# Kernel optimization log

Measured on AMD Instinct MI355X. Metric: run time of the kernel, lower is better.

Reference implementation:

```python
import jax, jax.numpy as jnp
import numpy as np

B, T, V, H, E, MAX_OOV = 128, 200, 50257, 256, 128, 50


def setup_inputs() -> dict:
    key = jax.random.key(0)
    ks = jax.random.split(key, 17)
    s = 0.05  # param scale
    return {
        "decoder_input": jax.random.randint(ks[0], (B, 1), 0, V),
        "encoder_outputs": jax.random.normal(ks[1], (B, T, 2 * H), jnp.float32),
        "encoder_idxs": jax.random.randint(ks[2], (B, T), 0, V),
        "prev_state": jax.random.normal(ks[3], (1, B, H), jnp.float32),
        "selective_read": jax.random.normal(ks[4], (B, 1, 2 * H), jnp.float32) * s,
        "step": 1,
        "emb": jax.random.normal(ks[5], (V, E), jnp.float32) * s,
        "W_ih": jax.random.normal(ks[6], (3 * H, E + 2 * H), jnp.float32) * s,
        "W_hh": jax.random.normal(ks[7], (3 * H, H), jnp.float32) * s,
        "b_ih": jax.random.normal(ks[8], (3 * H,), jnp.float32) * s,
        "b_hh": jax.random.normal(ks[9], (3 * H,), jnp.float32) * s,
        "Wi_w": jax.random.normal(ks[10], (H, 2 * H), jnp.float32) * s,
        "Wi_b": jax.random.normal(ks[11], (H,), jnp.float32) * s,
        "Wg_w": jax.random.normal(ks[12], (V, H), jnp.float32) * s,
        "Wg_b": jax.random.normal(ks[13], (V,), jnp.float32) * s,
        "Wc_w": jax.random.normal(ks[14], (H, 2 * H), jnp.float32) * s,
        "Wc_b": jax.random.normal(ks[15], (H,), jnp.float32) * s,
    }


def _gru_cell(x, h, W_ih, W_hh, b_ih, b_hh):
    # torch GRUCell math, gate order r,z,n
    gi = x @ W_ih.T + b_ih
    gh = h @ W_hh.T + b_hh
    i_r, i_z, i_n = jnp.split(gi, 3, axis=-1)
    h_r, h_z, h_n = jnp.split(gh, 3, axis=-1)
    r = jax.nn.sigmoid(i_r + h_r)
    z = jax.nn.sigmoid(i_z + h_z)
    n = jnp.tanh(i_n + r * h_n)
    return (1.0 - z) * n + z * h


def reference(decoder_input, encoder_outputs, encoder_idxs, prev_state, selective_read,
              step, emb, W_ih, W_hh, b_ih, b_hh, Wi_w, Wi_b, Wg_w, Wg_b, Wc_w, Wc_b):
    dtype = encoder_outputs.dtype
    if step == 0:
        prev_state = (encoder_outputs[:, -1] @ Wi_w.T + Wi_b)[None]      # 1,B,H
        selective_read = jnp.zeros((B, 1, 2 * H), dtype)
    embedded = emb[decoder_input[:, 0]]                                   # B,E
    gru_in = jnp.concatenate([selective_read[:, 0], embedded], axis=-1)   # B,2H+E
    decode_hidden = _gru_cell(gru_in, prev_state[0], W_ih, W_hh, b_ih, b_hh)  # B,H

    score_g = decode_hidden @ Wg_w.T + Wg_b                               # B,V
    enc_proj = jnp.tanh(jnp.einsum('bte,he->bth', encoder_outputs, Wc_w) + Wc_b)  # B,T,H
    score_c = jnp.tanh(jnp.einsum('bth,bh->bt', enc_proj, decode_hidden))         # B,T
    score_c = score_c + jnp.where(encoder_idxs == 0, -10000.0, 0.0).astype(dtype)

    probs = jax.nn.softmax(jnp.concatenate([score_g, score_c], axis=1), axis=1)   # B,V+T
    prob_g, prob_c = probs[:, :V], probs[:, V:]
    prob_g = jnp.concatenate([prob_g, jnp.full((B, MAX_OOV), 1e-4, dtype)], axis=1)  # B,V+oov

    # copy-distribution aggregation: scatter-add prob_c by vocab id (replaces one-hot bmm)
    prob_c_to_g = jnp.zeros((B, V + MAX_OOV), dtype).at[
        jnp.arange(B)[:, None], encoder_idxs].add(prob_c)
    prob_out = (prob_c_to_g + prob_g)[:, None, :]                          # B,1,V+oov

    # selective read for next step
    match = (encoder_idxs == decoder_input).astype(dtype)                  # B,T
    tot = match.sum(axis=1, keepdims=True)
    match = jnp.where(tot > 1, match / tot, match)
    prob_appeared = prob_c * match
    selective_read_new = jnp.einsum('bt,bte->be', prob_appeared, encoder_outputs)[:, None, :]  # B,1,2H
    return prob_out, decode_hidden, selective_read_new
```

## Files before the change

### kernel.cpp

```cpp
#include <hip/hip_runtime.h>

typedef __bf16 bf16;
typedef __bf16 bf16x8 __attribute__((ext_vector_type(8)));
typedef float f32x4 __attribute__((ext_vector_type(4)));

#define B_ 128
#define T_ 200
#define V_ 50257
#define H_ 256
#define E_ 128
#define OOV_ 50
#define VO_ 50307
#define NRG 80
#define NTS 5
#define GSC 629
#define TILES_G 3145
#define PSTR 3152
#define GPJ 400

__device__ __forceinline__ float sigmoid_(float x) { return 1.0f / (1.0f + __expf(-x)); }
__device__ __forceinline__ float tanh_(float x) { return 1.0f - 2.0f / (__expf(2.0f * x) + 1.0f); }

__global__ void k_front(const float* Wc_w, bf16* WcPack,
                        const int* step_p, const float* enc, const float* prev,
                        const float* selread, const int* dec, const float* emb,
                        const float* Wi_w, const float* Wi_b,
                        float* hT, float* ginT) {
    if (blockIdx.x < 128) {
        int gid = blockIdx.x * 256 + threadIdx.x;
        int n = gid >> 7;
        int k = (gid & 127) * 4;
        float4 v = *(const float4*)(Wc_w + n * 512 + k);
        int kstep = k >> 5, kin = k & 31;
        int q = kin >> 3, j0 = kin & 7;
        int r = n & 15, nt = n >> 4;
        int lane = q * 16 + r;
        bf16* d = WcPack + (((nt * 16 + kstep) * 64) + lane) * 8 + j0;
        d[0] = (bf16)v.x; d[1] = (bf16)v.y; d[2] = (bf16)v.z; d[3] = (bf16)v.w;
    } else {
        int b = blockIdx.x - 128, t = threadIdx.x;
        int step = step_p[0];
        float h;
        if (step == 0) {
            float acc = Wi_b[t];
            const float* er = enc + (b * T_ + (T_ - 1)) * 512;
            const float* wr = Wi_w + t * 512;
            for (int k = 0; k < 512; ++k) acc += er[k] * wr[k];
            h = acc;
        } else {
            h = prev[b * H_ + t];
        }
        hT[t * B_ + b] = h;
        for (int k = t; k < 512; k += 256)
            ginT[k * B_ + b] = (step == 0) ? 0.0f : selread[b * 512 + k];
        if (t < E_)
            ginT[(512 + t) * B_ + b] = emb[dec[b] * E_ + t];
    }
}

__global__ void k_gemm_gru(const float* W_ih, const float* b_ih,
                           const float* W_hh, const float* b_hh,
                           const float* ginT, const float* hT,
                           float* giT, float* ghT) {
    int g = blockIdx.x * 256 + threadIdx.x;
    int r = g >> 7, b = g & 127;
    const float* w = W_ih + r * 640;
    float a0 = 0.f, a1 = 0.f, a2 = 0.f, a3 = 0.f;
#pragma unroll 4
    for (int k = 0; k < 640; k += 4) {
        a0 += w[k]     * ginT[k * B_ + b];
        a1 += w[k + 1] * ginT[(k + 1) * B_ + b];
        a2 += w[k + 2] * ginT[(k + 2) * B_ + b];
        a3 += w[k + 3] * ginT[(k + 3) * B_ + b];
    }
    giT[r * B_ + b] = b_ih[r] + ((a0 + a1) + (a2 + a3));
    const float* w2 = W_hh + r * 256;
    float c0 = 0.f, c1 = 0.f, c2 = 0.f, c3 = 0.f;
#pragma unroll 4
    for (int k = 0; k < 256; k += 4) {
        c0 += w2[k]     * hT[k * B_ + b];
        c1 += w2[k + 1] * hT[(k + 1) * B_ + b];
        c2 += w2[k + 2] * hT[(k + 2) * B_ + b];
        c3 += w2[k + 3] * hT[(k + 3) * B_ + b];
    }
    ghT[r * B_ + b] = b_hh[r] + ((c0 + c1) + (c2 + c3));
}

__global__ void k_gru_cell(const float* giT, const float* ghT, const float* hT,
                           float* out_dh, bf16* Apack) {
    int b = blockIdx.x, j = threadIdx.x;
    float ir = giT[j * B_ + b], iz = giT[(256 + j) * B_ + b], in_ = giT[(512 + j) * B_ + b];
    float hr = ghT[j * B_ + b], hz = ghT[(256 + j) * B_ + b], hn = ghT[(512 + j) * B_ + b];
    float hp = hT[j * B_ + b];
    float r = sigmoid_(ir + hr);
    float z = sigmoid_(iz + hz);
    float n = tanh_(in_ + r * hn);
    float h = (1.0f - z) * n + z * hp;
    out_dh[b * H_ + j] = h;
    int mt = b >> 4, rr = b & 15, ks = j >> 5, q = (j >> 3) & 3, jj = j & 7;
    Apack[(((mt * 8 + ks) * 64) + (q * 16 + rr)) * 8 + jj] = (bf16)h;
}

__global__ __launch_bounds__(256, 3) void k_mm(const bf16* Apack, const float* Wg_w,
                                               const float* Wg_b, const float* enc,
                                               const bf16* WcPack, const float* Wc_b,
                                               const float* dh, const int* idxs,
                                               float* out_prob, float* pg_part, float* expc) {
    __shared__ unsigned char smem[43008];
    int tid = threadIdx.x;
    int w = tid >> 6, lane = tid & 63;
    int r = lane & 15, q = lane >> 4;
    if (blockIdx.x < GSC) {
        int blk = blockIdx.x;
        int n0 = blk * NRG;
        bf16* Bs = (bf16*)smem;
#pragma unroll
        for (int ph = 0; ph < 2; ++ph) {
            float4 tmp[10];
#pragma unroll
            for (int j = 0; j < 10; ++j) {
                int f = (ph * 10 + j) * 256 + tid;
                int row = f >> 6, c4 = f & 63;
                int n = n0 + row;
                tmp[j] = (n < V_) ? *(const float4*)(Wg_w + n * 256 + c4 * 4)
                                  : float4{0.f, 0.f, 0.f, 0.f};
            }
#pragma unroll
            for (int j = 0; j < 10; ++j) {
                int f = (ph * 10 + j) * 256 + tid;
                int row = f >> 6, c4 = f & 63;
                bf16* d = Bs + row * 264 + c4 * 4;
                d[0] = (bf16)tmp[j].x; d[1] = (bf16)tmp[j].y;
                d[2] = (bf16)tmp[j].z; d[3] = (bf16)tmp[j].w;
            }
        }
        bf16x8 a[2][8];
#pragma unroll
        for (int p = 0; p < 2; ++p)
#pragma unroll
            for (int ks = 0; ks < 8; ++ks)
                a[p][ks] = *(const bf16x8*)(Apack + ((2 * w + p) * 8 + ks) * 512 + lane * 8);
        __syncthreads();
        f32x4 acc[10];
#pragma unroll
        for (int i = 0; i < 10; ++i) acc[i] = (f32x4){0.f, 0.f, 0.f, 0.f};
#pragma unroll
        for (int ks = 0; ks < 8; ++ks) {
#pragma unroll
            for (int nt = 0; nt < NTS; ++nt) {
                bf16x8 bfr = *(const bf16x8*)(Bs + (nt * 16 + r) * 264 + ks * 32 + q * 8);
                acc[nt * 2]     = __builtin_amdgcn_mfma_f32_16x16x32_bf16(a[0][ks], bfr, acc[nt * 2], 0, 0, 0);
                acc[nt * 2 + 1] = __builtin_amdgcn_mfma_f32_16x16x32_bf16(a[1][ks], bfr, acc[nt * 2 + 1], 0, 0, 0);
            }
        }
        __syncthreads();
        float* Tr = (float*)smem;
#pragma unroll
        for (int nt = 0; nt < NTS; ++nt) {
            int n = n0 + nt * 16 + r;
            bool valid = n < V_;
            float wgb = valid ? Wg_b[n] : 0.0f;
#pragma unroll
            for (int p = 0; p < 2; ++p) {
#pragma unroll
                for (int rg = 0; rg < 4; ++rg) {
                    int row = (2 * w + p) * 16 + q * 4 + rg;
                    float e = valid ? __expf(acc[nt * 2 + p][rg] + wgb) : 0.0f;
                    Tr[row * 84 + nt * 16 + r] = e;
                    float sred = e;
                    sred += __shfl_xor(sred, 1);
                    sred += __shfl_xor(sred, 2);
                    sred += __shfl_xor(sred, 4);
                    sred += __shfl_xor(sred, 8);
                    if (r == 0) pg_part[row * PSTR + blk * NTS + nt] = sred;
                }
            }
        }
        __syncthreads();
        if (blk < GSC - 1) {
#pragma unroll
            for (int rnd = 0; rnd < 10; ++rnd) {
                int f = rnd * 256 + tid;
                int row = (f * 3277) >> 16;
                int c4 = f - row * 20;
                float4 v = *(const float4*)(Tr + row * 84 + c4 * 4);
                *(float4*)(out_prob + row * VO_ + n0 + c4 * 4) = v;
            }
        } else {
#pragma unroll
            for (int rnd = 0; rnd < 10; ++rnd) {
                int f = rnd * 256 + tid;
                int row = (f * 3277) >> 16;
                int c4 = f - row * 20;
#pragma unroll
                for (int i = 0; i < 4; ++i) {
                    int n = n0 + c4 * 4 + i;
                    if (n < V_) out_prob[row * VO_ + n] = Tr[row * 84 + c4 * 4 + i];
                }
            }
        }
    } else {
        int pblk = blockIdx.x - GSC;
        int m0 = pblk * 64;
        bf16* As = (bf16*)smem;
        float* sred = (float*)(smem + 33792);
        f32x4 acc[16];
#pragma unroll
        for (int i = 0; i < 16; ++i) acc[i] = (f32x4){0.f, 0.f, 0.f, 0.f};
        for (int half = 0; half < 2; ++half) {
            __syncthreads();
#pragma unroll
            for (int ph = 0; ph < 2; ++ph) {
                float4 tmp[8];
#pragma unroll
                for (int j = 0; j < 8; ++j) {
                    int f = (ph * 8 + j) * 256 + tid;
                    int row = f >> 6, c4 = f & 63;
                    tmp[j] = *(const float4*)(enc + (m0 + row) * 512 + half * 256 + c4 * 4);
                }
#pragma unroll
                for (int j = 0; j < 8; ++j) {
                    int f = (ph * 8 + j) * 256 + tid;
                    int row = f >> 6, c4 = f & 63;
                    bf16* d = As + row * 264 + c4 * 4;
                    d[0] = (bf16)tmp[j].x; d[1] = (bf16)tmp[j].y;
                    d[2] = (bf16)tmp[j].z; d[3] = (bf16)tmp[j].w;
                }
            }
            __syncthreads();
#pragma unroll
            for (int ks = 0; ks < 8; ++ks) {
                int kstep = half * 8 + ks;
                bf16x8 bfr[4];
#pragma unroll
                for (int ntl = 0; ntl < 4; ++ntl)
                    bfr[ntl] = *(const bf16x8*)(WcPack + (((w * 4 + ntl) * 16 + kstep) * 64 + lane) * 8);
#pragma unroll
                for (int mt = 0; mt < 4; ++mt) {
                    bf16x8 a = *(const bf16x8*)(As + (mt * 16 + r) * 264 + ks * 32 + q * 8);
#pragma unroll
                    for (int ntl = 0; ntl < 4; ++ntl)
                        acc[mt * 4 + ntl] = __builtin_amdgcn_mfma_f32_16x16x32_bf16(a, bfr[ntl], acc[mt * 4 + ntl], 0, 0, 0);
                }
            }
        }
#pragma unroll
        for (int mt = 0; mt < 4; ++mt) {
#pragma unroll
            for (int rg = 0; rg < 4; ++rg) {
                int rowl = mt * 16 + q * 4 + rg;
                int row = m0 + rowl;
                int b = row / T_;
                float s = 0.0f;
#pragma unroll
                for (int ntl = 0; ntl < 4; ++ntl) {
                    int n = (w * 4 + ntl) * 16 + r;
                    float pv = tanh_(acc[mt * 4 + ntl][rg] + Wc_b[n]);
                    s += pv * dh[b * H_ + n];
                }
                s += __shfl_xor(s, 1);
                s += __shfl_xor(s, 2);
                s += __shfl_xor(s, 4);
                s += __shfl_xor(s, 8);
                if (r == 0) sred[rowl * 4 + w] = s;
            }
        }
        __syncthreads();
        if (tid < 64) {
            float s = sred[tid * 4] + sred[tid * 4 + 1] + sred[tid * 4 + 2] + sred[tid * 4 + 3];
            int row = m0 + tid;
            int b = row / T_, t = row - b * T_;
            float sc = tanh_(s);
            if (idxs[b * T_ + t] == 0) sc -= 10000.0f;
            expc[row] = __expf(sc);
        }
    }
}

__global__ void k_red_scatter(const float* pg_part, const float* expc_, const int* idxs,
                              const int* dec, const float* enc, float* inv_out,
                              float* out_prob, float* out_sel) {
    __shared__ float red[256];
    __shared__ float cf[256];
    int b = blockIdx.x, t = threadIdx.x;
    float s = 0.0f;
    for (int i = t; i < TILES_G; i += 256) s += pg_part[b * PSTR + i];
    if (t < T_) s += expc_[b * T_ + t];
    red[t] = s;
    __syncthreads();
    for (int k = 128; k > 0; k >>= 1) {
        if (t < k) red[t] += red[t + k];
        __syncthreads();
    }
    float iv = 1.0f / red[0];
    if (t == 0) inv_out[b] = iv;
    __syncthreads();
    int d = dec[b];
    float ec = 0.0f;
    int m = 0;
    if (t < T_) {
        int ix = idxs[b * T_ + t];
        ec = expc_[b * T_ + t];
        atomicAdd(&out_prob[b * VO_ + ix], ec);
        m = (ix == d) ? 1 : 0;
    }
    cf[t] = m ? ec * iv : 0.0f;
    red[t] = m ? 1.0f : 0.0f;
    __syncthreads();
    for (int k = 128; k > 0; k >>= 1) {
        if (t < k) red[t] += red[t + k];
        __syncthreads();
    }
    float tot = red[0];
    float scale = (tot > 1.0f) ? 1.0f / tot : 1.0f;
    float a0 = 0.0f, a1 = 0.0f;
    for (int tt = 0; tt < T_; ++tt) {
        float c = cf[tt];
        if (c != 0.0f) {
            float wgt = c * scale;
            a0 += wgt * enc[(b * T_ + tt) * 512 + t];
            a1 += wgt * enc[(b * T_ + tt) * 512 + t + 256];
        }
    }
    out_sel[b * 512 + t] = a0;
    out_sel[b * 512 + t + 256] = a1;
}

__global__ void k_norm(float* out_prob, const float* inv) {
    int i4 = blockIdx.x * 256 + threadIdx.x;
    if (i4 >= (B_ * VO_ / 4)) return;
    float4 vv = ((const float4*)out_prob)[i4];
    float r[4];
    int base = i4 * 4;
#pragma unroll
    for (int c = 0; c < 4; ++c) {
        int idx = base + c;
        int b = idx / VO_;
        int v = idx - b * VO_;
        float x = (c == 0) ? vv.x : (c == 1) ? vv.y : (c == 2) ? vv.z : vv.w;
        r[c] = (v < V_) ? x * inv[b] : 1e-4f;
    }
    ((float4*)out_prob)[i4] = make_float4(r[0], r[1], r[2], r[3]);
}

extern "C" void kernel_launch(void* const* d_in, const int* in_sizes, int n_in,
                              void* d_out, int out_size, void* d_ws, size_t ws_size,
                              hipStream_t stream) {
    const int*   dec     = (const int*)d_in[0];
    const float* enc     = (const float*)d_in[1];
    const int*   idxs    = (const int*)d_in[2];
    const float* prev    = (const float*)d_in[3];
    const float* selread = (const float*)d_in[4];
    const int*   step_p  = (const int*)d_in[5];
    const float* emb     = (const float*)d_in[6];
    const float* W_ih    = (const float*)d_in[7];
    const float* W_hh    = (const float*)d_in[8];
    const float* b_ih    = (const float*)d_in[9];
    const float* b_hh    = (const float*)d_in[10];
    const float* Wi_w    = (const float*)d_in[11];
    const float* Wi_b    = (const float*)d_in[12];
    const float* Wg_w    = (const float*)d_in[13];
    const float* Wg_b    = (const float*)d_in[14];
    const float* Wc_w    = (const float*)d_in[15];
    const float* Wc_b    = (const float*)d_in[16];

    float* ws     = (float*)d_ws;
    float* hT     = ws;
    float* ginT   = ws + 32768;
    float* giT    = ws + 114688;
    float* ghT    = ws + 212992;
    float* inv    = ws + 311296;
    float* expc   = ws + 311552;
    float* pgp    = ws + 337152;
    bf16*  Apack  = (bf16*)(ws + 741376);
    bf16*  WcPack = (bf16*)(ws + 757760);

    float* out      = (float*)d_out;
    float* out_prob = out;
    float* out_dh   = out + 6439296;
    float* out_sel  = out + 6439296 + 32768;

    k_front<<<256, 256, 0, stream>>>(Wc_w, WcPack, step_p, enc, prev, selread, dec,
                                     emb, Wi_w, Wi_b, hT, ginT);
    k_gemm_gru<<<384, 256, 0, stream>>>(W_ih, b_ih, W_hh, b_hh, ginT, hT, giT, ghT);
    k_gru_cell<<<B_, 256, 0, stream>>>(giT, ghT, hT, out_dh, Apack);
    k_mm<<<GSC + GPJ, 256, 0, stream>>>(Apack, Wg_w, Wg_b, enc, WcPack, Wc_b,
                                        out_dh, idxs, out_prob, pgp, expc);
    k_red_scatter<<<B_, 256, 0, stream>>>(pgp, expc, idxs, dec, enc, inv, out_prob, out_sel);
    k_norm<<<(B_ * VO_ / 4 + 255) / 256, 256, 0, stream>>>(out_prob, inv);
}
```

Before: 276.2 us.

## Shrink vocab tiles, split GRU GEMM over K, vectorize bf16 smem stores

The vocab projection tile drops from 80 to 64 rows per block. This cuts LDS use so four blocks can fit per CU, and lets each block emit a single partial sum per row instead of one per 16-column subtile, which shortens the reduction in the scatter kernel. The GRU input/hidden GEMM now splits the K dimension across two thread halves and combines them through shared memory, doubling the grid size to raise parallelism. Global-to-LDS staging loads all tiles at once and writes bf16x4 vectors instead of scalar bf16 stores. The trade-off is more blocks and more register pressure from the larger staging arrays.

```diff
diff --git a/kernel.cpp b/kernel.cpp
--- a/kernel.cpp
+++ b/kernel.cpp
@@ -1,6 +1,7 @@
 #include <hip/hip_runtime.h>
 
 typedef __bf16 bf16;
+typedef __bf16 bf16x4 __attribute__((ext_vector_type(4)));
 typedef __bf16 bf16x8 __attribute__((ext_vector_type(8)));
 typedef float f32x4 __attribute__((ext_vector_type(4)));
 
@@ -11,11 +12,10 @@
 #define E_ 128
 #define OOV_ 50
 #define VO_ 50307
-#define NRG 80
-#define NTS 5
-#define GSC 629
-#define TILES_G 3145
-#define PSTR 3152
+#define NRG 64
+#define NTS 4
+#define GSC 786
+#define PSTR 800
 #define GPJ 400
 
 __device__ __forceinline__ float sigmoid_(float x) { return 1.0f / (1.0f + __expf(-x)); }
@@ -62,28 +62,37 @@
                            const float* W_hh, const float* b_hh,
                            const float* ginT, const float* hT,
                            float* giT, float* ghT) {
-    int g = blockIdx.x * 256 + threadIdx.x;
-    int r = g >> 7, b = g & 127;
-    const float* w = W_ih + r * 640;
+    __shared__ float red[256];
+    int rrow = blockIdx.x;
+    int t = threadIdx.x;
+    int b = t & 127, kh = t >> 7;
+    const float* w = W_ih + rrow * 640 + kh * 320;
+    const float* g = ginT + (kh * 320) * B_ + b;
     float a0 = 0.f, a1 = 0.f, a2 = 0.f, a3 = 0.f;
 #pragma unroll 4
-    for (int k = 0; k < 640; k += 4) {
-        a0 += w[k]     * ginT[k * B_ + b];
-        a1 += w[k + 1] * ginT[(k + 1) * B_ + b];
-        a2 += w[k + 2] * ginT[(k + 2) * B_ + b];
-        a3 += w[k + 3] * ginT[(k + 3) * B_ + b];
-    }
-    giT[r * B_ + b] = b_ih[r] + ((a0 + a1) + (a2 + a3));
-    const float* w2 = W_hh + r * 256;
+    for (int k = 0; k < 320; k += 4) {
+        a0 += w[k]     * g[k * B_];
+        a1 += w[k + 1] * g[(k + 1) * B_];
+        a2 += w[k + 2] * g[(k + 2) * B_];
+        a3 += w[k + 3] * g[(k + 3) * B_];
+    }
+    const float* w2 = W_hh + rrow * 256 + kh * 128;
+    const float* hh = hT + (kh * 128) * B_ + b;
     float c0 = 0.f, c1 = 0.f, c2 = 0.f, c3 = 0.f;
 #pragma unroll 4
-    for (int k = 0; k < 256; k += 4) {
-        c0 += w2[k]     * hT[k * B_ + b];
-        c1 += w2[k + 1] * hT[(k + 1) * B_ + b];
-        c2 += w2[k + 2] * hT[(k + 2) * B_ + b];
-        c3 += w2[k + 3] * hT[(k + 3) * B_ + b];
-    }
-    ghT[r * B_ + b] = b_hh[r] + ((c0 + c1) + (c2 + c3));
+    for (int k = 0; k < 128; k += 4) {
+        c0 += w2[k]     * hh[k * B_];
+        c1 += w2[k + 1] * hh[(k + 1) * B_];
+        c2 += w2[k + 2] * hh[(k + 2) * B_];
+        c3 += w2[k + 3] * hh[(k + 3) * B_];
+    }
+    red[t] = ((a0 + a1) + (a2 + a3));
+    __syncthreads();
+    if (kh == 0) giT[rrow * B_ + b] = b_ih[rrow] + red[b] + red[b + 128];
+    __syncthreads();
+    red[t] = ((c0 + c1) + (c2 + c3));
+    __syncthreads();
+    if (kh == 0) ghT[rrow * B_ + b] = b_hh[rrow] + red[b] + red[b + 128];
 }
 
 __global__ void k_gru_cell(const float* giT, const float* ghT, const float* hT,
@@ -101,12 +110,12 @@
     Apack[(((mt * 8 + ks) * 64) + (q * 16 + rr)) * 8 + jj] = (bf16)h;
 }
 
-__global__ __launch_bounds__(256, 3) void k_mm(const bf16* Apack, const float* Wg_w,
+__global__ __launch_bounds__(256, 4) void k_mm(const bf16* Apack, const float* Wg_w,
                                                const float* Wg_b, const float* enc,
                                                const bf16* WcPack, const float* Wc_b,
                                                const float* dh, const int* idxs,
                                                float* out_prob, float* pg_part, float* expc) {
-    __shared__ unsigned char smem[43008];
+    __shared__ unsigned char smem[34816];
     int tid = threadIdx.x;
     int w = tid >> 6, lane = tid & 63;
     int r = lane & 15, q = lane >> 4;
@@ -114,25 +123,23 @@
         int blk = blockIdx.x;
         int n0 = blk * NRG;
         bf16* Bs = (bf16*)smem;
-#pragma unroll
-        for (int ph = 0; ph < 2; ++ph) {
-            float4 tmp[10];
-#pragma unroll
-            for (int j = 0; j < 10; ++j) {
-                int f = (ph * 10 + j) * 256 + tid;
-                int row = f >> 6, c4 = f & 63;
-                int n = n0 + row;
-                tmp[j] = (n < V_) ? *(const float4*)(Wg_w + n * 256 + c4 * 4)
-                                  : float4{0.f, 0.f, 0.f, 0.f};
-            }
-#pragma unroll
-            for (int j = 0; j < 10; ++j) {
-                int f = (ph * 10 + j) * 256 + tid;
-                int row = f >> 6, c4 = f & 63;
-                bf16* d = Bs + row * 264 + c4 * 4;
-                d[0] = (bf16)tmp[j].x; d[1] = (bf16)tmp[j].y;
-                d[2] = (bf16)tmp[j].z; d[3] = (bf16)tmp[j].w;
-            }
+        float4 tmp[16];
+#pragma unroll
+        for (int j = 0; j < 16; ++j) {
+            int f = j * 256 + tid;
+            int row = f >> 6, c4 = f & 63;
+            int n = n0 + row;
+            tmp[j] = (n < V_) ? *(const float4*)(Wg_w + n * 256 + c4 * 4)
+                              : float4{0.f, 0.f, 0.f, 0.f};
+        }
+#pragma unroll
+        for (int j = 0; j < 16; ++j) {
+            int f = j * 256 + tid;
+            int row = f >> 6, c4 = f & 63;
+            bf16x4 o;
+            o[0] = (bf16)tmp[j].x; o[1] = (bf16)tmp[j].y;
+            o[2] = (bf16)tmp[j].z; o[3] = (bf16)tmp[j].w;
+            *(bf16x4*)(Bs + row * 264 + c4 * 4) = o;
         }
         bf16x8 a[2][8];
 #pragma unroll
@@ -141,9 +148,9 @@
             for (int ks = 0; ks < 8; ++ks)
                 a[p][ks] = *(const bf16x8*)(Apack + ((2 * w + p) * 8 + ks) * 512 + lane * 8);
         __syncthreads();
-        f32x4 acc[10];
-#pragma unroll
-        for (int i = 0; i < 10; ++i) acc[i] = (f32x4){0.f, 0.f, 0.f, 0.f};
+        f32x4 acc[8];
+#pragma unroll
+        for (int i = 0; i < 8; ++i) acc[i] = (f32x4){0.f, 0.f, 0.f, 0.f};
 #pragma unroll
         for (int ks = 0; ks < 8; ++ks) {
 #pragma unroll
@@ -155,6 +162,11 @@
         }
         __syncthreads();
         float* Tr = (float*)smem;
+        float rsum[2][4];
+#pragma unroll
+        for (int p = 0; p < 2; ++p)
+#pragma unroll
+            for (int rg = 0; rg < 4; ++rg) rsum[p][rg] = 0.0f;
 #pragma unroll
         for (int nt = 0; nt < NTS; ++nt) {
             int n = n0 + nt * 16 + r;
@@ -166,36 +178,46 @@
                 for (int rg = 0; rg < 4; ++rg) {
                     int row = (2 * w + p) * 16 + q * 4 + rg;
                     float e = valid ? __expf(acc[nt * 2 + p][rg] + wgb) : 0.0f;
-                    Tr[row * 84 + nt * 16 + r] = e;
-                    float sred = e;
-                    sred += __shfl_xor(sred, 1);
-                    sred += __shfl_xor(sred, 2);
-                    sred += __shfl_xor(sred, 4);
-                    sred += __shfl_xor(sred, 8);
-                    if (r == 0) pg_part[row * PSTR + blk * NTS + nt] = sred;
+                    Tr[row * 68 + nt * 16 + r] = e;
+                    rsum[p][rg] += e;
                 }
             }
         }
+#pragma unroll
+        for (int p = 0; p < 2; ++p) {
+#pragma unroll
+            for (int rg = 0; rg < 4; ++rg) {
+                float s = rsum[p][rg];
+                s += __shfl_xor(s, 1);
+                s += __shfl_xor(s, 2);
+                s += __shfl_xor(s, 4);
+                s += __shfl_xor(s, 8);
+                if (r == 0) {
+                    int row = (2 * w + p) * 16 + q * 4 + rg;
+                    pg_part[row * PSTR + blk] = s;
+                }
+            }
+        }
         __syncthreads();
         if (blk < GSC - 1) {
 #pragma unroll
-            for (int rnd = 0; rnd < 10; ++rnd) {
+            for (int rnd = 0; rnd < 8; ++rnd) {
                 int f = rnd * 256 + tid;
-                int row = (f * 3277) >> 16;
-                int c4 = f - row * 20;
-                float4 v = *(const float4*)(Tr + row * 84 + c4 * 4);
+                int row = f >> 4;
+                int c4 = f & 15;
+                float4 v = *(const float4*)(Tr + row * 68 + c4 * 4);
                 *(float4*)(out_prob + row * VO_ + n0 + c4 * 4) = v;
             }
         } else {
 #pragma unroll
-            for (int rnd = 0; rnd < 10; ++rnd) {
+            for (int rnd = 0; rnd < 8; ++rnd) {
                 int f = rnd * 256 + tid;
-                int row = (f * 3277) >> 16;
-                int c4 = f - row * 20;
+                int row = f >> 4;
+                int c4 = f & 15;
 #pragma unroll
                 for (int i = 0; i < 4; ++i) {
                     int n = n0 + c4 * 4 + i;
-                    if (n < V_) out_prob[row * VO_ + n] = Tr[row * 84 + c4 * 4 + i];
+                    if (n < V_) out_prob[row * VO_ + n] = Tr[row * 68 + c4 * 4 + i];
                 }
             }
         }
@@ -209,23 +231,21 @@
         for (int i = 0; i < 16; ++i) acc[i] = (f32x4){0.f, 0.f, 0.f, 0.f};
         for (int half = 0; half < 2; ++half) {
             __syncthreads();
-#pragma unroll
-            for (int ph = 0; ph < 2; ++ph) {
-                float4 tmp[8];
-#pragma unroll
-                for (int j = 0; j < 8; ++j) {
-                    int f = (ph * 8 + j) * 256 + tid;
-                    int row = f >> 6, c4 = f & 63;
-                    tmp[j] = *(const float4*)(enc + (m0 + row) * 512 + half * 256 + c4 * 4);
-                }
-#pragma unroll
-                for (int j = 0; j < 8; ++j) {
-                    int f = (ph * 8 + j) * 256 + tid;
-                    int row = f >> 6, c4 = f & 63;
-                    bf16* d = As + row * 264 + c4 * 4;
-                    d[0] = (bf16)tmp[j].x; d[1] = (bf16)tmp[j].y;
-                    d[2] = (bf16)tmp[j].z; d[3] = (bf16)tmp[j].w;
-                }
+            float4 tmp[16];
+#pragma unroll
+            for (int j = 0; j < 16; ++j) {
+                int f = j * 256 + tid;
+                int row = f >> 6, c4 = f & 63;
+                tmp[j] = *(const float4*)(enc + (m0 + row) * 512 + half * 256 + c4 * 4);
+            }
+#pragma unroll
+            for (int j = 0; j < 16; ++j) {
+                int f = j * 256 + tid;
+                int row = f >> 6, c4 = f & 63;
+                bf16x4 o;
+                o[0] = (bf16)tmp[j].x; o[1] = (bf16)tmp[j].y;
+                o[2] = (bf16)tmp[j].z; o[3] = (bf16)tmp[j].w;
+                *(bf16x4*)(As + row * 264 + c4 * 4) = o;
             }
             __syncthreads();
 #pragma unroll
@@ -284,7 +304,7 @@
     __shared__ float cf[256];
     int b = blockIdx.x, t = threadIdx.x;
     float s = 0.0f;
-    for (int i = t; i < TILES_G; i += 256) s += pg_part[b * PSTR + i];
+    for (int i = t; i < GSC; i += 256) s += pg_part[b * PSTR + i];
     if (t < T_) s += expc_[b * T_ + t];
     red[t] = s;
     __syncthreads();
@@ -382,7 +402,7 @@
 
     k_front<<<256, 256, 0, stream>>>(Wc_w, WcPack, step_p, enc, prev, selread, dec,
                                      emb, Wi_w, Wi_b, hT, ginT);
-    k_gemm_gru<<<384, 256, 0, stream>>>(W_ih, b_ih, W_hh, b_hh, ginT, hT, giT, ghT);
+    k_gemm_gru<<<768, 256, 0, stream>>>(W_ih, b_ih, W_hh, b_hh, ginT, hT, giT, ghT);
     k_gru_cell<<<B_, 256, 0, stream>>>(giT, ghT, hT, out_dh, Apack);
     k_mm<<<GSC + GPJ, 256, 0, stream>>>(Apack, Wg_w, Wg_b, enc, WcPack, Wc_b,
                                         out_dh, idxs, out_prob, pgp, expc);
```

After: 282.3 us. 1.02x slower.
